# Kernel tuning notes

Hardware: AMD Instinct MI355X
Metric: run time of the kernel (lower is better)

Reference implementation:

```python
import jax, jax.numpy as jnp
import numpy as np

N_NODES = 50000
N_EDGES = 600000
IN_DIM = 128
HID = 128


def setup_inputs() -> dict:
    key = jax.random.key(0)
    ks = jax.random.split(key, 8)
    x = jax.random.normal(ks[0], (N_NODES, IN_DIM), dtype=jnp.float32)
    edge_index = jax.random.randint(ks[1], (2, N_EDGES), 0, N_NODES, dtype=jnp.int64)
    def lin(k, fan_in, fan_out):
        s = 1.0 / np.sqrt(fan_in)
        kw, kb = jax.random.split(k)
        W = jax.random.uniform(kw, (fan_in, fan_out), jnp.float32, -s, s)
        b = jax.random.uniform(kb, (fan_out,), jnp.float32, -s, s)
        return W, b
    W0, b0 = lin(ks[2], IN_DIM, HID)
    W1, b1 = lin(ks[3], HID, HID)
    W2, b2 = lin(ks[4], HID, HID)
    return {"x": x, "edge_index": edge_index, "W0": W0, "b0": b0,
            "W1": W1, "b1": b1, "W2": W2, "b2": b2}


def reference(x, edge_index, W0, b0, W1, b1, W2, b2):
    n = x.shape[0]
    loops = jnp.arange(n, dtype=edge_index.dtype)
    src = jnp.concatenate([edge_index[0], loops])  # source nodes (+self loops)
    dst = jnp.concatenate([edge_index[1], loops])  # destination nodes
    # symmetric GCN normalization: deg^{-1/2}[src] * deg^{-1/2}[dst]
    deg = jax.ops.segment_sum(jnp.ones(src.shape[0], x.dtype), dst, num_segments=n)
    dinv = jnp.where(deg > 0, jax.lax.rsqrt(deg), 0.0)
    norm = dinv[src] * dinv[dst]  # [E+N]

    def gcn_layer(h, W, b):
        hw = h @ W                              # [N, H]
        msg = hw[src] * norm[:, None]           # gather + scale, [E+N, H]
        agg = jax.ops.segment_sum(msg, dst, num_segments=n)  # scatter-add
        return agg + b

    h = x
    for W, b in ((W0, b0), (W1, b1), (W2, b2)):
        h = jax.nn.relu(gcn_layer(h, W, b))     # dropout is identity in eval
    return h  # JK='last'
```

## Files before the change

### kernel.cpp

```cpp
#include <hip/hip_runtime.h>

#define NN 50000
#define NE 600000
#define DIM 128
#define NB_N 196
#define NB_E 2344
#define TILES 3125
#define ROWW 136
#define NEPAD (NE + 4 * NN + 64)

typedef unsigned short u16;
typedef unsigned int u32;
typedef __attribute__((ext_vector_type(8))) short bf16x8;
typedef __attribute__((ext_vector_type(4))) float f32x4;

__device__ __forceinline__ u16 f2bf(float f) {
    u32 u = __builtin_bit_cast(u32, f);
    u32 r = (u + 0x7FFFu + ((u >> 16) & 1u)) >> 16;
    return (u16)r;
}
__device__ __forceinline__ float bflo(u32 w) { return __builtin_bit_cast(float, w << 16); }
__device__ __forceinline__ float bfhi(u32 w) { return __builtin_bit_cast(float, w & 0xffff0000u); }
__device__ __forceinline__ float i2f(int b) { return __builtin_bit_cast(float, b); }


__global__ __launch_bounds__(256) void k_count(const int* __restrict__ ei,
                                               int* __restrict__ deg) {
    __shared__ int s64;
    if (threadIdx.x == 0) {
        int o = 0;
#pragma unroll
        for (int j = 0; j < 16; j++) o |= ei[2 * j + 1];
        s64 = (o == 0);
    }
    __syncthreads();
    int e = blockIdx.x * 256 + threadIdx.x;
    if (e >= NE) return;
    int d = s64 ? ei[2 * (NE + e)] : ei[NE + e];
    atomicAdd(&deg[d], 1);
}

__device__ __forceinline__ int pad4(int d) {
    int p = (d + 3) & ~3;
    return p < 4 ? 4 : p;
}

__global__ __launch_bounds__(256) void k_scanA(const int* __restrict__ deg,
                                               int* __restrict__ rp4,
                                               int* __restrict__ bsum) {
    __shared__ int buf[256];
    int t = threadIdx.x, i = blockIdx.x * 256 + t;
    int v = (i < NN) ? pad4(deg[i]) : 0;
    buf[t] = v;
    __syncthreads();
    for (int off = 1; off < 256; off <<= 1) {
        int x = (t >= off) ? buf[t - off] : 0;
        __syncthreads();
        buf[t] += x;
        __syncthreads();
    }
    if (i < NN) rp4[i] = buf[t] - v;
    if (t == 255) bsum[blockIdx.x] = buf[255];
}

__global__ __launch_bounds__(256) void k_scanB(int* __restrict__ bsum) {
    __shared__ int buf[256];
    int t = threadIdx.x;
    int v = (t < NB_N) ? bsum[t] : 0;
    buf[t] = v;
    __syncthreads();
    for (int off = 1; off < 256; off <<= 1) {
        int x = (t >= off) ? buf[t - off] : 0;
        __syncthreads();
        buf[t] += x;
        __syncthreads();
    }
    bsum[t] = buf[t] - v;
}

__global__ __launch_bounds__(256) void k_scanC(const int* __restrict__ deg,
                                               int* __restrict__ rp4,
                                               const int* __restrict__ bsum,
                                               float* __restrict__ dinv,
                                               int2* __restrict__ recs) {
    int i = blockIdx.x * 256 + threadIdx.x;
    if (i < NN) {
        int rp = rp4[i] + bsum[i >> 8];
        rp4[i] = rp;
        int d = deg[i];
        dinv[i] = rsqrtf((float)(d + 1));
        int p = pad4(d);
        for (int j = d; j < p; j++) recs[rp + j] = make_int2(0, 0);
    }
    if (i == 0) rp4[NN] = bsum[255];
}

__global__ __launch_bounds__(256) void k_fill(const int* __restrict__ ei,
                                              const int* __restrict__ rp4,
                                              int* __restrict__ cursor,
                                              const float* __restrict__ dinv,
                                              int2* __restrict__ recs) {
    __shared__ int s64;
    if (threadIdx.x == 0) {
        int o = 0;
#pragma unroll
        for (int j = 0; j < 16; j++) o |= ei[2 * j + 1];
        s64 = (o == 0);
    }
    __syncthreads();
    int e = blockIdx.x * 256 + threadIdx.x;
    if (e >= NE) return;
    int is64 = s64;
    int s = is64 ? ei[2 * e] : ei[e];
    int d = is64 ? ei[2 * (NE + e)] : ei[NE + e];
    int pos = rp4[d] + atomicAdd(&cursor[d], 1);
    int2 rc;
    rc.x = s;
    rc.y = __builtin_bit_cast(int, dinv[s] * dinv[d]);
    recs[pos] = rc;
}

__global__ __launch_bounds__(256) void k_wcast(const float* __restrict__ W0,
                                               const float* __restrict__ W1,
                                               const float* __restrict__ W2,
                                               u16* __restrict__ Wt) {
    int idx = blockIdx.x * 256 + threadIdx.x;
    int l = idx >> 14, rem = idx & 16383;
    int n = rem >> 7, k = rem & 127;
    const float* W = (l == 0) ? W0 : ((l == 1) ? W1 : W2);
    Wt[idx] = f2bf(W[k * 128 + n]);
}

__global__ __launch_bounds__(256) void k_gemm_f32(const float* __restrict__ x,
                                                  const u16* __restrict__ Wt,
                                                  u16* __restrict__ hwb) {
    int lane = threadIdx.x & 63;
    int tile = blockIdx.x * 4 + (threadIdx.x >> 6);
    if (tile >= TILES) return;
    int r = lane & 15, q = lane >> 4;

    bf16x8 Bf[8][4];
#pragma unroll
    for (int nt = 0; nt < 8; nt++)
#pragma unroll
        for (int kc = 0; kc < 4; kc++)
            Bf[nt][kc] = *(const bf16x8*)(Wt + ((nt * 16 + r) << 7) + kc * 32 + q * 8);

    long rowbase = (long)tile * 16;
    bf16x8 Af[4];
#pragma unroll
    for (int kc = 0; kc < 4; kc++) {
        const float4* p = (const float4*)(x + (rowbase + r) * 128 + kc * 32 + q * 8);
        float4 t0 = p[0], t1 = p[1];
        bf16x8 a;
        a[0] = (short)f2bf(t0.x); a[1] = (short)f2bf(t0.y);
        a[2] = (short)f2bf(t0.z); a[3] = (short)f2bf(t0.w);
        a[4] = (short)f2bf(t1.x); a[5] = (short)f2bf(t1.y);
        a[6] = (short)f2bf(t1.z); a[7] = (short)f2bf(t1.w);
        Af[kc] = a;
    }

#pragma unroll
    for (int nt = 0; nt < 8; nt++) {
        f32x4 acc = {0.f, 0.f, 0.f, 0.f};
#pragma unroll
        for (int kc = 0; kc < 4; kc++)
            acc = __builtin_amdgcn_mfma_f32_16x16x32_bf16(Af[kc], Bf[nt][kc], acc, 0, 0, 0);
#pragma unroll
        for (int i = 0; i < 4; i++)
            hwb[(rowbase + q * 4 + i) * 128 + nt * 16 + r] = f2bf(acc[i]);
    }
}

__device__ __forceinline__ void fma8(float* acc, uint4 u, float n) {
    acc[0] += n * bflo(u.x); acc[1] += n * bfhi(u.x);
    acc[2] += n * bflo(u.y); acc[3] += n * bfhi(u.y);
    acc[4] += n * bflo(u.z); acc[5] += n * bfhi(u.z);
    acc[6] += n * bflo(u.w); acc[7] += n * bfhi(u.w);
}

__device__ __forceinline__ void combine_bias_relu(float b0x, float b0y, float b0z,
                                                  float b0w, float b1x, float b1y,
                                                  float b1z, float b1w, float* acc) {
#pragma unroll
    for (int j = 0; j < 8; j++) {
        acc[j] += __shfl_xor(acc[j], 16, 64);
        acc[j] += __shfl_xor(acc[j], 32, 64);
    }
    acc[0] = fmaxf(acc[0] + b0x, 0.f); acc[1] = fmaxf(acc[1] + b0y, 0.f);
    acc[2] = fmaxf(acc[2] + b0z, 0.f); acc[3] = fmaxf(acc[3] + b0w, 0.f);
    acc[4] = fmaxf(acc[4] + b1x, 0.f); acc[5] = fmaxf(acc[5] + b1y, 0.f);
    acc[6] = fmaxf(acc[6] + b1z, 0.f); acc[7] = fmaxf(acc[7] + b1w, 0.f);
}

__device__ __forceinline__ void agg_quad(const u16* __restrict__ hw,
                                         const int* __restrict__ rp4,
                                         const int2* __restrict__ recs,
                                         const float* __restrict__ dinv,
                                         int vbase, int g, int r,
                                         float A[4][8]) {
    int4 rlo = *(const int4*)(rp4 + vbase);
    int rhi = rp4[vbase + 4];
    int s0 = rlo.x, s1 = rlo.y, s2 = rlo.z, s3 = rlo.w;
    int l0 = rlo.y - rlo.x, l1 = rlo.z - rlo.y, l2 = rlo.w - rlo.z, l3 = rhi - rlo.w;

    uint4 sv = *(const uint4*)(hw + (size_t)(vbase + g) * DIM + r * 8);
    float4 dv4 = *(const float4*)(dinv + vbase);
    float dvg = (g == 0) ? dv4.x : (g == 1) ? dv4.y : (g == 2) ? dv4.z : dv4.w;
    float sc = dvg * dvg;

    int2 q0 = recs[s0 + g], q1 = recs[s1 + g], q2 = recs[s2 + g], q3 = recs[s3 + g];

#pragma unroll
    for (int c = 0; c < 4; c++) {
        float s = (g == c) ? sc : 0.f;
        A[c][0] = s * bflo(sv.x); A[c][1] = s * bfhi(sv.x);
        A[c][2] = s * bflo(sv.y); A[c][3] = s * bfhi(sv.y);
        A[c][4] = s * bflo(sv.z); A[c][5] = s * bfhi(sv.z);
        A[c][6] = s * bflo(sv.w); A[c][7] = s * bfhi(sv.w);
    }

    int nit = max(max(l0, l1), max(l2, l3)) >> 2;
    for (int it = 0; it < nit; ++it) {
        uint4 u0 = *(const uint4*)(hw + (size_t)(u32)q0.x * DIM + r * 8);
        uint4 u1 = *(const uint4*)(hw + (size_t)(u32)q1.x * DIM + r * 8);
        uint4 u2 = *(const uint4*)(hw + (size_t)(u32)q2.x * DIM + r * 8);
        uint4 u3 = *(const uint4*)(hw + (size_t)(u32)q3.x * DIM + r * 8);
        int nx = 4 * (it + 1);
        int2 p0 = recs[s0 + min(nx, l0 - 4) + g];
        int2 p1 = recs[s1 + min(nx, l1 - 4) + g];
        int2 p2 = recs[s2 + min(nx, l2 - 4) + g];
        int2 p3 = recs[s3 + min(nx, l3 - 4) + g];
        int cur = 4 * it;
        float n0 = (cur < l0) ? i2f(q0.y) : 0.f;
        float n1 = (cur < l1) ? i2f(q1.y) : 0.f;
        float n2 = (cur < l2) ? i2f(q2.y) : 0.f;
        float n3 = (cur < l3) ? i2f(q3.y) : 0.f;
        fma8(A[0], u0, n0);
        fma8(A[1], u1, n1);
        fma8(A[2], u2, n2);
        fma8(A[3], u3, n3);
        q0 = p0; q1 = p1; q2 = p2; q3 = p3;
    }
}

__global__ __launch_bounds__(256) void k_agg_gemm(const u16* __restrict__ hw_in,
                                                  const int* __restrict__ rp4,
                                                  const int2* __restrict__ recs,
                                                  const float* __restrict__ dinv,
                                                  const float* __restrict__ bias,
                                                  const u16* __restrict__ Wt,
                                                  u16* __restrict__ hw_out) {
    __shared__ u16 sm[16 * ROWW];
    int lane = threadIdx.x & 63;
    int w = threadIdx.x >> 6;
    int g = lane >> 4, r = lane & 15;
    int base = blockIdx.x * 16;
    int vbase = base + w * 4;

    float4 b0 = ((const float4*)bias)[2 * r];
    float4 b1 = ((const float4*)bias)[2 * r + 1];

    float A[4][8];
    agg_quad(hw_in, rp4, recs, dinv, vbase, g, r, A);
#pragma unroll
    for (int c = 0; c < 4; c++) {
        combine_bias_relu(b0.x, b0.y, b0.z, b0.w, b1.x, b1.y, b1.z, b1.w, A[c]);
        if (g == c) {
            uint4 pk;
            pk.x = (u32)f2bf(A[c][0]) | ((u32)f2bf(A[c][1]) << 16);
            pk.y = (u32)f2bf(A[c][2]) | ((u32)f2bf(A[c][3]) << 16);
            pk.z = (u32)f2bf(A[c][4]) | ((u32)f2bf(A[c][5]) << 16);
            pk.w = (u32)f2bf(A[c][6]) | ((u32)f2bf(A[c][7]) << 16);
            *(uint4*)(sm + (w * 4 + c) * ROWW + r * 8) = pk;
        }
    }
    __syncthreads();
    int q = lane >> 4;
    bf16x8 Af[4];
#pragma unroll
    for (int kc = 0; kc < 4; kc++)
        Af[kc] = *(const bf16x8*)(sm + r * ROWW + kc * 32 + q * 8);
#pragma unroll
    for (int t = 0; t < 2; t++) {
        int nt = w * 2 + t;
        f32x4 acc = {0.f, 0.f, 0.f, 0.f};
#pragma unroll
        for (int kc = 0; kc < 4; kc++) {
            bf16x8 Bf = *(const bf16x8*)(Wt + ((nt * 16 + r) << 7) + kc * 32 + q * 8);
            acc = __builtin_amdgcn_mfma_f32_16x16x32_bf16(Af[kc], Bf, acc, 0, 0, 0);
        }
#pragma unroll
        for (int i = 0; i < 4; i++)
            hw_out[(size_t)(base + q * 4 + i) * DIM + nt * 16 + r] = f2bf(acc[i]);
    }
}

__global__ __launch_bounds__(256) void k_agg_out(const u16* __restrict__ hw_in,
                                                 const int* __restrict__ rp4,
                                                 const int2* __restrict__ recs,
                                                 const float* __restrict__ dinv,
                                                 const float* __restrict__ bias,
                                                 float* __restrict__ out) {
    int lane = threadIdx.x & 63;
    int w = threadIdx.x >> 6;
    int g = lane >> 4, r = lane & 15;
    int vbase = blockIdx.x * 16 + w * 4;

    float4 b0 = ((const float4*)bias)[2 * r];
    float4 b1 = ((const float4*)bias)[2 * r + 1];

    float A[4][8];
    agg_quad(hw_in, rp4, recs, dinv, vbase, g, r, A);
#pragma unroll
    for (int c = 0; c < 4; c++) {
        combine_bias_relu(b0.x, b0.y, b0.z, b0.w, b1.x, b1.y, b1.z, b1.w, A[c]);
        if (g == c) {
            float4* p = (float4*)(out + (size_t)(vbase + c) * DIM + r * 8);
            p[0] = make_float4(A[c][0], A[c][1], A[c][2], A[c][3]);
            p[1] = make_float4(A[c][4], A[c][5], A[c][6], A[c][7]);
        }
    }
}


extern "C" void kernel_launch(void* const* d_in, const int* in_sizes, int n_in,
                              void* d_out, int out_size, void* d_ws, size_t ws_size,
                              hipStream_t stream) {
    const float* x = (const float*)d_in[0];
    const int* ei = (const int*)d_in[1];
    const float* W0 = (const float*)d_in[2];
    const float* b0 = (const float*)d_in[3];
    const float* W1 = (const float*)d_in[4];
    const float* b1 = (const float*)d_in[5];
    const float* W2 = (const float*)d_in[6];
    const float* b2 = (const float*)d_in[7];

    char* ws = (char*)d_ws;
    size_t off = 0;
    auto alloc = [&](size_t bytes) -> void* {
        void* p = ws + off;
        off += (bytes + 511) & ~(size_t)511;
        return p;
    };
    int* deg = (int*)alloc(NN * 4);
    int* cursor = (int*)alloc(NN * 4);
    size_t zbytes = off;
    int2* recs = (int2*)alloc((size_t)NEPAD * 8);
    float* dinv = (float*)alloc(NN * 4);
    int* rp4 = (int*)alloc((NN + 1) * 4);
    int* bsum = (int*)alloc(256 * 4);
    u16* Wt = (u16*)alloc(3 * 128 * 128 * 2);
    u16* hwA = (u16*)alloc((size_t)NN * DIM * 2);
    u16* hwB = (u16*)alloc((size_t)NN * DIM * 2);

    hipMemsetAsync(ws, 0, zbytes, stream);
    k_count<<<NB_E, 256, 0, stream>>>(ei, deg);
    k_scanA<<<NB_N, 256, 0, stream>>>(deg, rp4, bsum);
    k_scanB<<<1, 256, 0, stream>>>(bsum);
    k_scanC<<<NB_N, 256, 0, stream>>>(deg, rp4, bsum, dinv, recs);
    k_fill<<<NB_E, 256, 0, stream>>>(ei, rp4, cursor, dinv, recs);
    k_wcast<<<192, 256, 0, stream>>>(W0, W1, W2, Wt);

    k_gemm_f32<<<(TILES + 3) / 4, 256, 0, stream>>>(x, Wt, hwA);
    k_agg_gemm<<<TILES, 256, 0, stream>>>(hwA, rp4, recs, dinv, b0,
                                          Wt + 16384, hwB);
    k_agg_gemm<<<TILES, 256, 0, stream>>>(hwB, rp4, recs, dinv, b1,
                                          Wt + 32768, hwA);
    k_agg_out<<<TILES, 256, 0, stream>>>(hwA, rp4, recs, dinv, b2,
                                         (float*)d_out);
}
```

Measured before the change: 290.5 us.

## Split aggregation into feature-sliced passes and unfuse GEMM into separate kernel

Aggregation is now split into 4 passes over 32-feature slices, with each wave's 16-lane group handling one node and 4 lanes per edge slot. Partial sums are reduced by shuffles before bias, ReLU and store. The dense transform that was fused via shared memory is moved into a separate GEMM kernel that reads the bf16 aggregated features. This aims to raise parallelism and shrink per-thread register state in the gather loop. The cost is 4x more blocks, repeated index and record loads per pass, and an extra global round-trip of the intermediate activations between kernels.

```diff
diff --git a/kernel.cpp b/kernel.cpp
--- a/kernel.cpp
+++ b/kernel.cpp
@@ -6,7 +6,6 @@
 #define NB_N 196
 #define NB_E 2344
 #define TILES 3125
-#define ROWW 136
 #define NEPAD (NE + 4 * NN + 64)
 
 typedef unsigned short u16;
@@ -172,153 +171,108 @@
     }
 }
 
-__device__ __forceinline__ void fma8(float* acc, uint4 u, float n) {
-    acc[0] += n * bflo(u.x); acc[1] += n * bfhi(u.x);
-    acc[2] += n * bflo(u.y); acc[3] += n * bfhi(u.y);
-    acc[4] += n * bflo(u.z); acc[5] += n * bfhi(u.z);
-    acc[6] += n * bflo(u.w); acc[7] += n * bfhi(u.w);
-}
-
-__device__ __forceinline__ void combine_bias_relu(float b0x, float b0y, float b0z,
-                                                  float b0w, float b1x, float b1y,
-                                                  float b1z, float b1w, float* acc) {
-#pragma unroll
-    for (int j = 0; j < 8; j++) {
-        acc[j] += __shfl_xor(acc[j], 16, 64);
-        acc[j] += __shfl_xor(acc[j], 32, 64);
-    }
-    acc[0] = fmaxf(acc[0] + b0x, 0.f); acc[1] = fmaxf(acc[1] + b0y, 0.f);
-    acc[2] = fmaxf(acc[2] + b0z, 0.f); acc[3] = fmaxf(acc[3] + b0w, 0.f);
-    acc[4] = fmaxf(acc[4] + b1x, 0.f); acc[5] = fmaxf(acc[5] + b1y, 0.f);
-    acc[6] = fmaxf(acc[6] + b1z, 0.f); acc[7] = fmaxf(acc[7] + b1w, 0.f);
-}
-
-__device__ __forceinline__ void agg_quad(const u16* __restrict__ hw,
-                                         const int* __restrict__ rp4,
-                                         const int2* __restrict__ recs,
-                                         const float* __restrict__ dinv,
-                                         int vbase, int g, int r,
-                                         float A[4][8]) {
+__global__ __launch_bounds__(256) void k_gemm(const u16* __restrict__ hb,
+                                              const u16* __restrict__ Wt,
+                                              u16* __restrict__ hwb) {
+    int lane = threadIdx.x & 63;
+    int tile = blockIdx.x * 4 + (threadIdx.x >> 6);
+    if (tile >= TILES) return;
+    int r = lane & 15, q = lane >> 4;
+
+    bf16x8 Bf[8][4];
+#pragma unroll
+    for (int nt = 0; nt < 8; nt++)
+#pragma unroll
+        for (int kc = 0; kc < 4; kc++)
+            Bf[nt][kc] = *(const bf16x8*)(Wt + ((nt * 16 + r) << 7) + kc * 32 + q * 8);
+
+    long rowbase = (long)tile * 16;
+    bf16x8 Af[4];
+#pragma unroll
+    for (int kc = 0; kc < 4; kc++)
+        Af[kc] = *(const bf16x8*)(hb + ((rowbase + r) << 7) + kc * 32 + q * 8);
+
+#pragma unroll
+    for (int nt = 0; nt < 8; nt++) {
+        f32x4 acc = {0.f, 0.f, 0.f, 0.f};
+#pragma unroll
+        for (int kc = 0; kc < 4; kc++)
+            acc = __builtin_amdgcn_mfma_f32_16x16x32_bf16(Af[kc], Bf[nt][kc], acc, 0, 0, 0);
+#pragma unroll
+        for (int i = 0; i < 4; i++)
+            hwb[(rowbase + q * 4 + i) * 128 + nt * 16 + r] = f2bf(acc[i]);
+    }
+}
+
+__global__ __launch_bounds__(256) void k_agg4(const u16* __restrict__ hw_in,
+                                              const int* __restrict__ rp4,
+                                              const int2* __restrict__ recs,
+                                              const float* __restrict__ dinv,
+                                              const float* __restrict__ bias,
+                                              u16* __restrict__ bf_out,
+                                              float* __restrict__ f_out,
+                                              int write_f32) {
+    int pass = blockIdx.x / TILES;
+    int tile = blockIdx.x - pass * TILES;
+    int lane = threadIdx.x & 63;
+    int w = threadIdx.x >> 6;
+    int chain = lane >> 4, e4 = (lane >> 2) & 3, fq = lane & 3;
+    int vbase = tile * 16 + w * 4;
+    int base16 = pass * 32 + fq * 8;
+
     int4 rlo = *(const int4*)(rp4 + vbase);
     int rhi = rp4[vbase + 4];
-    int s0 = rlo.x, s1 = rlo.y, s2 = rlo.z, s3 = rlo.w;
-    int l0 = rlo.y - rlo.x, l1 = rlo.z - rlo.y, l2 = rlo.w - rlo.z, l3 = rhi - rlo.w;
-
-    uint4 sv = *(const uint4*)(hw + (size_t)(vbase + g) * DIM + r * 8);
-    float4 dv4 = *(const float4*)(dinv + vbase);
-    float dvg = (g == 0) ? dv4.x : (g == 1) ? dv4.y : (g == 2) ? dv4.z : dv4.w;
-    float sc = dvg * dvg;
-
-    int2 q0 = recs[s0 + g], q1 = recs[s1 + g], q2 = recs[s2 + g], q3 = recs[s3 + g];
-
-#pragma unroll
-    for (int c = 0; c < 4; c++) {
-        float s = (g == c) ? sc : 0.f;
-        A[c][0] = s * bflo(sv.x); A[c][1] = s * bfhi(sv.x);
-        A[c][2] = s * bflo(sv.y); A[c][3] = s * bfhi(sv.y);
-        A[c][4] = s * bflo(sv.z); A[c][5] = s * bfhi(sv.z);
-        A[c][6] = s * bflo(sv.w); A[c][7] = s * bfhi(sv.w);
-    }
-
-    int nit = max(max(l0, l1), max(l2, l3)) >> 2;
+    int s_c = (chain == 0) ? rlo.x : (chain == 1) ? rlo.y : (chain == 2) ? rlo.z : rlo.w;
+    int nxt = (chain == 0) ? rlo.y : (chain == 1) ? rlo.z : (chain == 2) ? rlo.w : rhi;
+    int l_c = nxt - s_c;
+    int l_max = max(max(rlo.y - rlo.x, rlo.z - rlo.y), max(rlo.w - rlo.z, rhi - rlo.w));
+
+    uint4 sv = *(const uint4*)(hw_in + (size_t)(vbase + chain) * DIM + base16);
+    float dv = dinv[vbase + chain];
+    float sc = (e4 == 0) ? dv * dv : 0.0f;
+    float acc[8];
+    acc[0] = sc * bflo(sv.x); acc[1] = sc * bfhi(sv.x);
+    acc[2] = sc * bflo(sv.y); acc[3] = sc * bfhi(sv.y);
+    acc[4] = sc * bflo(sv.z); acc[5] = sc * bfhi(sv.z);
+    acc[6] = sc * bflo(sv.w); acc[7] = sc * bfhi(sv.w);
+
+    int nit = l_max >> 2;
     for (int it = 0; it < nit; ++it) {
-        uint4 u0 = *(const uint4*)(hw + (size_t)(u32)q0.x * DIM + r * 8);
-        uint4 u1 = *(const uint4*)(hw + (size_t)(u32)q1.x * DIM + r * 8);
-        uint4 u2 = *(const uint4*)(hw + (size_t)(u32)q2.x * DIM + r * 8);
-        uint4 u3 = *(const uint4*)(hw + (size_t)(u32)q3.x * DIM + r * 8);
-        int nx = 4 * (it + 1);
-        int2 p0 = recs[s0 + min(nx, l0 - 4) + g];
-        int2 p1 = recs[s1 + min(nx, l1 - 4) + g];
-        int2 p2 = recs[s2 + min(nx, l2 - 4) + g];
-        int2 p3 = recs[s3 + min(nx, l3 - 4) + g];
-        int cur = 4 * it;
-        float n0 = (cur < l0) ? i2f(q0.y) : 0.f;
-        float n1 = (cur < l1) ? i2f(q1.y) : 0.f;
-        float n2 = (cur < l2) ? i2f(q2.y) : 0.f;
-        float n3 = (cur < l3) ? i2f(q3.y) : 0.f;
-        fma8(A[0], u0, n0);
-        fma8(A[1], u1, n1);
-        fma8(A[2], u2, n2);
-        fma8(A[3], u3, n3);
-        q0 = p0; q1 = p1; q2 = p2; q3 = p3;
-    }
-}
-
-__global__ __launch_bounds__(256) void k_agg_gemm(const u16* __restrict__ hw_in,
-                                                  const int* __restrict__ rp4,
-                                                  const int2* __restrict__ recs,
-                                                  const float* __restrict__ dinv,
-                                                  const float* __restrict__ bias,
-                                                  const u16* __restrict__ Wt,
-                                                  u16* __restrict__ hw_out) {
-    __shared__ u16 sm[16 * ROWW];
-    int lane = threadIdx.x & 63;
-    int w = threadIdx.x >> 6;
-    int g = lane >> 4, r = lane & 15;
-    int base = blockIdx.x * 16;
-    int vbase = base + w * 4;
-
-    float4 b0 = ((const float4*)bias)[2 * r];
-    float4 b1 = ((const float4*)bias)[2 * r + 1];
-
-    float A[4][8];
-    agg_quad(hw_in, rp4, recs, dinv, vbase, g, r, A);
-#pragma unroll
-    for (int c = 0; c < 4; c++) {
-        combine_bias_relu(b0.x, b0.y, b0.z, b0.w, b1.x, b1.y, b1.z, b1.w, A[c]);
-        if (g == c) {
+        int eoff = 4 * it;
+        int idx = s_c + min(eoff, l_c - 4) + e4;
+        int2 rc = recs[idx];
+        uint4 u = *(const uint4*)(hw_in + (size_t)(u32)rc.x * DIM + base16);
+        float n = (eoff < l_c) ? i2f(rc.y) : 0.0f;
+        acc[0] += n * bflo(u.x); acc[1] += n * bfhi(u.x);
+        acc[2] += n * bflo(u.y); acc[3] += n * bfhi(u.y);
+        acc[4] += n * bflo(u.z); acc[5] += n * bfhi(u.z);
+        acc[6] += n * bflo(u.w); acc[7] += n * bfhi(u.w);
+    }
+
+#pragma unroll
+    for (int j = 0; j < 8; j++) {
+        acc[j] += __shfl_xor(acc[j], 4, 64);
+        acc[j] += __shfl_xor(acc[j], 8, 64);
+    }
+
+    if (e4 == 0) {
+        float4 b0 = ((const float4*)bias)[pass * 8 + fq * 2];
+        float4 b1 = ((const float4*)bias)[pass * 8 + fq * 2 + 1];
+        acc[0] = fmaxf(acc[0] + b0.x, 0.f); acc[1] = fmaxf(acc[1] + b0.y, 0.f);
+        acc[2] = fmaxf(acc[2] + b0.z, 0.f); acc[3] = fmaxf(acc[3] + b0.w, 0.f);
+        acc[4] = fmaxf(acc[4] + b1.x, 0.f); acc[5] = fmaxf(acc[5] + b1.y, 0.f);
+        acc[6] = fmaxf(acc[6] + b1.z, 0.f); acc[7] = fmaxf(acc[7] + b1.w, 0.f);
+        if (write_f32) {
+            float4* p = (float4*)(f_out + (size_t)(vbase + chain) * DIM + base16);
+            p[0] = make_float4(acc[0], acc[1], acc[2], acc[3]);
+            p[1] = make_float4(acc[4], acc[5], acc[6], acc[7]);
+        } else {
             uint4 pk;
-            pk.x = (u32)f2bf(A[c][0]) | ((u32)f2bf(A[c][1]) << 16);
-            pk.y = (u32)f2bf(A[c][2]) | ((u32)f2bf(A[c][3]) << 16);
-            pk.z = (u32)f2bf(A[c][4]) | ((u32)f2bf(A[c][5]) << 16);
-            pk.w = (u32)f2bf(A[c][6]) | ((u32)f2bf(A[c][7]) << 16);
-            *(uint4*)(sm + (w * 4 + c) * ROWW + r * 8) = pk;
-        }
-    }
-    __syncthreads();
-    int q = lane >> 4;
-    bf16x8 Af[4];
-#pragma unroll
-    for (int kc = 0; kc < 4; kc++)
-        Af[kc] = *(const bf16x8*)(sm + r * ROWW + kc * 32 + q * 8);
-#pragma unroll
-    for (int t = 0; t < 2; t++) {
-        int nt = w * 2 + t;
-        f32x4 acc = {0.f, 0.f, 0.f, 0.f};
-#pragma unroll
-        for (int kc = 0; kc < 4; kc++) {
-            bf16x8 Bf = *(const bf16x8*)(Wt + ((nt * 16 + r) << 7) + kc * 32 + q * 8);
-            acc = __builtin_amdgcn_mfma_f32_16x16x32_bf16(Af[kc], Bf, acc, 0, 0, 0);
-        }
-#pragma unroll
-        for (int i = 0; i < 4; i++)
-            hw_out[(size_t)(base + q * 4 + i) * DIM + nt * 16 + r] = f2bf(acc[i]);
-    }
-}
-
-__global__ __launch_bounds__(256) void k_agg_out(const u16* __restrict__ hw_in,
-                                                 const int* __restrict__ rp4,
-                                                 const int2* __restrict__ recs,
-                                                 const float* __restrict__ dinv,
-                                                 const float* __restrict__ bias,
-                                                 float* __restrict__ out) {
-    int lane = threadIdx.x & 63;
-    int w = threadIdx.x >> 6;
-    int g = lane >> 4, r = lane & 15;
-    int vbase = blockIdx.x * 16 + w * 4;
-
-    float4 b0 = ((const float4*)bias)[2 * r];
-    float4 b1 = ((const float4*)bias)[2 * r + 1];
-
-    float A[4][8];
-    agg_quad(hw_in, rp4, recs, dinv, vbase, g, r, A);
-#pragma unroll
-    for (int c = 0; c < 4; c++) {
-        combine_bias_relu(b0.x, b0.y, b0.z, b0.w, b1.x, b1.y, b1.z, b1.w, A[c]);
-        if (g == c) {
-            float4* p = (float4*)(out + (size_t)(vbase + c) * DIM + r * 8);
-            p[0] = make_float4(A[c][0], A[c][1], A[c][2], A[c][3]);
-            p[1] = make_float4(A[c][4], A[c][5], A[c][6], A[c][7]);
+            pk.x = (u32)f2bf(acc[0]) | ((u32)f2bf(acc[1]) << 16);
+            pk.y = (u32)f2bf(acc[2]) | ((u32)f2bf(acc[3]) << 16);
+            pk.z = (u32)f2bf(acc[4]) | ((u32)f2bf(acc[5]) << 16);
+            pk.w = (u32)f2bf(acc[6]) | ((u32)f2bf(acc[7]) << 16);
+            *(uint4*)(bf_out + (size_t)(vbase + chain) * DIM + base16) = pk;
         }
     }
 }
@@ -352,7 +306,7 @@
     int* bsum = (int*)alloc(256 * 4);
     u16* Wt = (u16*)alloc(3 * 128 * 128 * 2);
     u16* hwA = (u16*)alloc((size_t)NN * DIM * 2);
-    u16* hwB = (u16*)alloc((size_t)NN * DIM * 2);
+    u16* hB = (u16*)alloc((size_t)NN * DIM * 2);
 
     hipMemsetAsync(ws, 0, zbytes, stream);
     k_count<<<NB_E, 256, 0, stream>>>(ei, deg);
@@ -363,10 +317,12 @@
     k_wcast<<<192, 256, 0, stream>>>(W0, W1, W2, Wt);
 
     k_gemm_f32<<<(TILES + 3) / 4, 256, 0, stream>>>(x, Wt, hwA);
-    k_agg_gemm<<<TILES, 256, 0, stream>>>(hwA, rp4, recs, dinv, b0,
-                                          Wt + 16384, hwB);
-    k_agg_gemm<<<TILES, 256, 0, stream>>>(hwB, rp4, recs, dinv, b1,
-                                          Wt + 32768, hwA);
-    k_agg_out<<<TILES, 256, 0, stream>>>(hwA, rp4, recs, dinv, b2,
-                                         (float*)d_out);
-}
+    k_agg4<<<4 * TILES, 256, 0, stream>>>(hwA, rp4, recs, dinv, b0,
+                                          hB, nullptr, 0);
+    k_gemm<<<(TILES + 3) / 4, 256, 0, stream>>>(hB, Wt + 16384, hwA);
+    k_agg4<<<4 * TILES, 256, 0, stream>>>(hwA, rp4, recs, dinv, b1,
+                                          hB, nullptr, 0);
+    k_gemm<<<(TILES + 3) / 4, 256, 0, stream>>>(hB, Wt + 32768, hwA);
+    k_agg4<<<4 * TILES, 256, 0, stream>>>(hwA, rp4, recs, dinv, b2,
+                                          nullptr, (float*)d_out, 1);
+}
```

Result: slower. 339.7 us (+16.9%).
